# Optimization experiments

Hardware: AMD Instinct MI355X
Metric: run time of the kernel (lower is better)

The kernel has to match this reference:

```python
import jax, jax.numpy as jnp
import numpy as np

D = 128
RANK = 16
N_USER, N_PROD, N_CAT, N_BRAND = 100000, 100000, 1000, 2000
E_BEH, E_STR = 100000, 50000
NODE_TYPES = ['user', 'product', 'category', 'brand']
N_NODES = {'user': N_USER, 'product': N_PROD, 'category': N_CAT, 'brand': N_BRAND}
PHI = {'user': 0, 'product': 1, 'category': 2, 'brand': 3}
# (src_type, edge_name, dst_type, rel_idx, beta or None for structural)
EDGE_META = [
    ('user', 'view', 'product', 0, 0),
    ('user', 'cart', 'product', 1, 1),
    ('user', 'purchase', 'product', 2, 2),
    ('product', 'rev_view', 'user', 3, 0),
    ('product', 'rev_cart', 'user', 4, 1),
    ('product', 'rev_purchase', 'user', 5, 2),
    ('product', 'belongs_to', 'category', 6, None),
    ('category', 'contains', 'product', 7, None),
    ('product', 'producedBy', 'brand', 8, None),
    ('brand', 'brands', 'product', 9, None),
]


def setup_inputs() -> dict:
    key = jax.random.key(0)
    ks = iter(jax.random.split(key, 64))
    inp = {}
    for t in NODE_TYPES:
        inp['x_' + t] = jax.random.normal(next(ks), (N_NODES[t], D), jnp.float32)
    for (st, name, dt, ridx, beta) in EDGE_META:
        E = E_BEH if beta is not None else E_STR
        src = jax.random.randint(next(ks), (E,), 0, N_NODES[st], jnp.int32)
        dst = jax.random.randint(next(ks), (E,), 0, N_NODES[dt], jnp.int32)
        inp['ei_' + name] = jnp.stack([src, dst])
        if beta is None:
            inp['attr_' + name] = jax.random.randint(next(ks), (E,), 0, 3, jnp.int32)
    s = 0.05
    inp['W_base'] = jax.random.normal(next(ks), (D, D), jnp.float32) * s
    inp['A'] = jax.random.normal(next(ks), (4, D, RANK), jnp.float32) * s
    inp['B'] = jax.random.normal(next(ks), (4, D, RANK), jnp.float32) * s
    inp['rel_W'] = jax.random.normal(next(ks), (10, D), jnp.float32) * s
    inp['beh_W'] = jax.random.normal(next(ks), (4, D), jnp.float32) * s
    inp['a_att'] = jax.random.normal(next(ks), (4 * D,), jnp.float32) * s
    inp['ln_gamma'] = jnp.ones((D,), jnp.float32)
    inp['ln_beta'] = jnp.zeros((D,), jnp.float32)
    return inp


def _forward(x, eis, attrs, W_base, A, B, rel_W, beh_W, a_att, ln_gamma, ln_beta):
    a0, a1, a2, a3 = a_att[:D], a_att[D:2 * D], a_att[2 * D:3 * D], a_att[3 * D:]
    agg = {t: jnp.zeros((N_NODES[t], D), x['user'].dtype) for t in NODE_TYPES}
    for (src_t, name, dst_t, ridx, beta) in EDGE_META:
        ei = eis[name]
        src, dst = ei[0], ei[1]
        hs = x[src_t][src]            # [E, D] gather
        hd = x[dst_t][dst]            # [E, D] gather
        phi = PHI[src_t]
        if beta is not None:
            # uniform behavior beta: W = W_base + A_phi @ B_beta^T
            W = W_base + A[phi] @ B[beta].T
            msg = hs @ W.T
            hproj = hd @ W.T
            b_term = (beh_W[beta] * a3).sum()
        else:
            # per-edge behavior origin from edge_attr (clamped to {0,1,2})
            origin = jnp.clip(attrs[name].reshape(-1), 0, 2)
            mids = jnp.einsum('ei,bir->ebr', hs, B[:3])            # [E, 3, rank]
            mid = jnp.take_along_axis(mids, origin[:, None, None], axis=1)[:, 0, :]
            msg = hs @ W_base.T + mid @ A[phi].T
            hproj = hd @ W_base.T
            b_term = (beh_W[origin] * a3).sum(-1)                  # [E]
        r_scalar = (rel_W[ridx] * a2).sum()
        e = (msg * a0).sum(-1) + (hproj * a1).sum(-1) + r_scalar + b_term
        # destination-grouped softmax over edges
        n_dst = N_NODES[dst_t]
        m = jax.ops.segment_max(e, dst, num_segments=n_dst)
        ex = jnp.exp(e - m[dst])
        ssum = jax.ops.segment_sum(ex, dst, num_segments=n_dst)
        alpha = ex / (ssum[dst] + 1e-16)
        agg[dst_t] = agg[dst_t] + jax.ops.segment_sum(alpha[:, None] * msg, dst, num_segments=n_dst)
    outs = []
    for t in NODE_TYPES:
        h = agg[t]
        mu = h.mean(-1, keepdims=True)
        var = ((h - mu) ** 2).mean(-1, keepdims=True)
        hn = (h - mu) / jnp.sqrt(var + 1e-5) * ln_gamma + ln_beta
        outs.append(jax.nn.elu(hn + x[t]))   # residual: in_dim == out_dim
    return jnp.concatenate(outs, axis=0)     # [N_user+N_prod+N_cat+N_brand, D]


def reference(x_user, x_product, x_category, x_brand,
              ei_view, ei_cart, ei_purchase, ei_rev_view, ei_rev_cart, ei_rev_purchase,
              ei_belongs_to, ei_contains, ei_producedBy, ei_brands,
              attr_belongs_to, attr_contains, attr_producedBy, attr_brands,
              W_base, A, B, rel_W, beh_W, a_att, ln_gamma, ln_beta):
    x = {'user': x_user, 'product': x_product, 'category': x_category, 'brand': x_brand}
    eis = {'view': ei_view, 'cart': ei_cart, 'purchase': ei_purchase,
           'rev_view': ei_rev_view, 'rev_cart': ei_rev_cart, 'rev_purchase': ei_rev_purchase,
           'belongs_to': ei_belongs_to, 'contains': ei_contains,
           'producedBy': ei_producedBy, 'brands': ei_brands}
    attrs = {'belongs_to': attr_belongs_to, 'contains': attr_contains,
             'producedBy': attr_producedBy, 'brands': attr_brands}
    return _forward(x, eis, attrs, W_base, A, B, rel_W, beh_W, a_att, ln_gamma, ln_beta)
```

## Files before the change

### kernel.cpp

```cpp
#include <hip/hip_runtime.h>
#include <hip/hip_bf16.h>
#include <math.h>

#define D 128

#define NU 100000
#define NP 100000
#define NC 1000
#define NB 2000
#define NTOT 203000
#define EB 100000
#define ES 50000
#define ETOT 800000
#define NSEG 803000
#define NBLK 785

#define OFF_L    0
#define OFF_W0   6448000
#define OFF_BS   6451840
#define OFF_WT   7251856
#define OFF_AT   7268240
#define OFF_INT  7276432

__constant__ int c_srcT[10]   = {0,0,0,1,1,1,1,2,1,3};
__constant__ int c_phi [10]   = {0,0,0,1,1,1,1,2,1,3};
__constant__ int c_beta[10]   = {0,1,2,0,1,2,-1,-1,-1,-1};
__constant__ int c_E   [10]   = {EB,EB,EB,EB,EB,EB,ES,ES,ES,ES};
__constant__ int c_moff[10]   = {0,100000,200000,300000,400000,500000,600000,601000,701000,703000};

__constant__ int g_nGrp[4]    = {1,3,1,1};
__constant__ int g_Loff[4][3] = {{1600000,0,0},{0,3216000,4848000},{3200000,0,0},{4816000,0,0}};
__constant__ int g_ai[4][3]   = {{1,0,0},{0,2,3},{1,0,0},{1,0,0}};

#define K4_BU 782
#define K4_BP 1564
#define K4_BC 1572
#define K4_BT 1588

struct Ptrs {
    const float* x[4];
    const int*   ei[10];
    const int*   attr[4];
};

__device__ __forceinline__ void decode_et(int eflat, int& et, int& le) {
    if (eflat < 600000) { et = eflat / 100000; le = eflat - et * 100000; }
    else { int r = eflat - 600000; int q = r / 50000; et = 6 + q; le = r - q * 50000; }
}

__device__ __forceinline__ float qsum(float v) {
    v += __shfl_xor(v, 1, 64);
    v += __shfl_xor(v, 2, 64);
    v += __shfl_xor(v, 4, 64);
    v += __shfl_xor(v, 8, 64);
    return v;
}

__global__ void k0_tables(const float* __restrict__ Wb, const float* __restrict__ A,
                          const float* __restrict__ B, const float* __restrict__ behW,
                          const float* __restrict__ a_att,
                          float* __restrict__ w0, float* __restrict__ bs_out)
{
    __shared__ float a0[128];
    __shared__ float c0[128];
    __shared__ float g0[4][16];
    int t = threadIdx.x;
    if (t < 128) a0[t] = a_att[t];
    __syncthreads();
    if (t < 128) {
        float s0=0.f;
        for (int j=0;j<128;j++) s0 += Wb[j*128+t]*a0[j];
        c0[t]=s0;
    } else if (t < 192) {
        int q=t-128, p=q>>4, r=q&15;
        float s0=0.f;
        for (int i=0;i<128;i++) s0 += A[p*2048+i*16+r]*a0[i];
        g0[p][r]=s0;
    } else if (t < 196) {
        int b=t-192; float s=0.f;
        for (int i=0;i<128;i++) s += behW[b*128+i]*a_att[384+i];
        bs_out[b]=s;
    }
    __syncthreads();
    if (t < 128) {
        for (int et=0; et<10; ++et) {
            int phi=c_phi[et], beta=c_beta[et];
            if (beta >= 0) {
                float s0=c0[t];
                for (int r=0;r<16;r++) s0 += B[beta*2048+t*16+r]*g0[phi][r];
                w0[et*384+t]=s0; w0[et*384+128+t]=s0; w0[et*384+256+t]=s0;
            } else {
                for (int o=0;o<3;o++){
                    float s0=c0[t];
                    for (int r=0;r<16;r++) s0 += B[o*2048+t*16+r]*g0[phi][r];
                    w0[et*384+o*128+t]=s0;
                }
            }
        }
    }
}

__global__ __launch_bounds__(256) void ktrans(const float* __restrict__ Wb,
        const float* __restrict__ A, float* __restrict__ WbT, float* __restrict__ AT)
{
    int idx = blockIdx.x*256 + threadIdx.x;
    if (idx < 16384) { int i = idx>>7, j = idx&127; WbT[i*128+j] = Wb[j*128+i]; }
    int idx2 = idx - 16384;
    if (idx2 >= 0 && idx2 < 8192) {
        int p = idx2>>11, rem = idx2&2047, r = rem>>7, j = rem&127;
        AT[idx2] = A[p*2048 + j*16 + r];
    }
}

__global__ __launch_bounds__(256) void khist(Ptrs P, int* __restrict__ counts)
{
    int eflat = blockIdx.x*256 + threadIdx.x;
    if (eflat >= ETOT) return;
    int et, le; decode_et(eflat, et, le);
    int dst = P.ei[et][c_E[et] + le];
    atomicAdd(&counts[c_moff[et] + dst], 1);
}

__global__ __launch_bounds__(256) void kscan1(const int* __restrict__ cnt,
                                              int* __restrict__ st, int* __restrict__ bsums)
{
    __shared__ int lds[256];
    int t = threadIdx.x, b = blockIdx.x;
    int base = b*1024 + t*4;
    int v0 = (base   < NSEG) ? cnt[base]   : 0;
    int v1 = (base+1 < NSEG) ? cnt[base+1] : 0;
    int v2 = (base+2 < NSEG) ? cnt[base+2] : 0;
    int v3 = (base+3 < NSEG) ? cnt[base+3] : 0;
    int s = v0+v1+v2+v3;
    lds[t] = s; __syncthreads();
    for (int off=1; off<256; off<<=1){
        int xv = (t>=off) ? lds[t-off] : 0;
        __syncthreads();
        lds[t] += xv;
        __syncthreads();
    }
    int incl = lds[t];
    int p = incl - s;
    if (t==255) bsums[b] = incl;
    if (base   < NSEG) st[base]   = p; p += v0;
    if (base+1 < NSEG) st[base+1] = p; p += v1;
    if (base+2 < NSEG) st[base+2] = p; p += v2;
    if (base+3 < NSEG) st[base+3] = p;
}

__global__ __launch_bounds__(256) void kscan2(int* __restrict__ bsums)
{
    __shared__ int lds[256];
    int t = threadIdx.x;
    int base = t*4;
    int v0 = (base   < NBLK) ? bsums[base]   : 0;
    int v1 = (base+1 < NBLK) ? bsums[base+1] : 0;
    int v2 = (base+2 < NBLK) ? bsums[base+2] : 0;
    int v3 = (base+3 < NBLK) ? bsums[base+3] : 0;
    int s = v0+v1+v2+v3;
    lds[t] = s; __syncthreads();
    for (int off=1; off<256; off<<=1){
        int xv = (t>=off) ? lds[t-off] : 0;
        __syncthreads();
        lds[t] += xv;
        __syncthreads();
    }
    int p = lds[t] - s;
    if (base   < NBLK) bsums[base]   = p; p += v0;
    if (base+1 < NBLK) bsums[base+1] = p; p += v1;
    if (base+2 < NBLK) bsums[base+2] = p; p += v2;
    if (base+3 < NBLK) bsums[base+3] = p;
}

__global__ __launch_bounds__(256) void kscan3(int* __restrict__ st, const int* __restrict__ bsums)
{
    int t = threadIdx.x, b = blockIdx.x;
    int add = bsums[b];
    int base = b*1024 + t*4;
    #pragma unroll
    for (int j=0;j<4;j++)
        if (base+j < NSEG) st[base+j] += add;
}

__global__ __launch_bounds__(256) void kscatter(Ptrs P, int* __restrict__ st, int* __restrict__ srco)
{
    int eflat = blockIdx.x*256 + threadIdx.x;
    if (eflat >= ETOT) return;
    int et, le; decode_et(eflat, et, le);
    const int* ei = P.ei[et];
    int E = c_E[et];
    int src = ei[le], dst = ei[E+le];
    int o;
    if (et >= 6) { int a = P.attr[et-6][le]; o = min(max(a,0),2); }
    else o = c_beta[et];
    int pos = atomicAdd(&st[c_moff[et] + dst], 1);
    srco[pos] = src | (o<<17) | (et<<19);
}

__global__ __launch_bounds__(256) void kagg_beh(Ptrs P,
        const int* __restrict__ starts, const int* __restrict__ counts,
        const int* __restrict__ srco,
        const float* __restrict__ w0, const float* __restrict__ Bm,
        float* __restrict__ Sout, float* __restrict__ Lb, int nWaves)
{
    int lane = threadIdx.x & 63;
    int wv = (blockIdx.x * 256 + threadIdx.x) >> 6;
    int grp = lane >> 4, ln = lane & 15;

    for (int nid = wv; nid < NU + NP; nid += nWaves) {
        int T = (nid < NU) ? 0 : 1;
        int n0 = (T == 0) ? nid : nid - NU;
        int etBase = (T == 0) ? 3 : 0;
        const float* xs = P.x[1 - T];

        int sgA = c_moff[etBase] + n0;
        int cnt0 = counts[sgA],        cnt1 = counts[sgA+100000], cnt2 = counts[sgA+200000];
        int sa0  = starts[sgA]-cnt0,   sa1  = starts[sgA+100000]-cnt1, sa2 = starts[sgA+200000]-cnt2;
        int sv1 = (grp < cnt1) ? srco[sa1+grp] : 0;
        int sv2 = (grp < cnt2) ? srco[sa2+grp] : 0;
        float4 pA = make_float4(0.f,0.f,0.f,0.f), pB = pA;
        if (grp < cnt0) {
            int sv0 = srco[sa0+grp];
            const float* q = xs + (size_t)(sv0 & 0x1FFFF)*D + ln*8;
            pA = *(const float4*)q; pB = *(const float4*)(q+4);
        }

        float Stot[8] = {0,0,0,0,0,0,0,0};
        float Lq0=0.f, Lq1=0.f, Lq2=0.f, Lq3=0.f;

        for (int s=0; s<3; ++s) {
            int cnt = (s==0)?cnt0:((s==1)?cnt1:cnt2);
            int st0 = (s==0)?sa0:((s==1)?sa1:sa2);
            float4 cA = pA, cB = pB;
            pA = make_float4(0.f,0.f,0.f,0.f); pB = pA;
            if (s == 0) {
                if (grp < cnt1) {
                    const float* q = xs + (size_t)(sv1 & 0x1FFFF)*D + ln*8;
                    pA = *(const float4*)q; pB = *(const float4*)(q+4);
                }
            } else if (s == 1) {
                if (grp < cnt2) {
                    const float* q = xs + (size_t)(sv2 & 0x1FFFF)*D + ln*8;
                    pA = *(const float4*)q; pB = *(const float4*)(q+4);
                }
            }
            if (cnt == 0) continue;
            int et = etBase + s;
            const float* wq = w0 + et*384 + ln*8;
            float4 wA = *(const float4*)wq, wB = *(const float4*)(wq+4);

            float ssum = 0.f;
            float SA[8] = {0,0,0,0,0,0,0,0};

            for (int k0=0; k0<cnt; k0+=4) {
                bool act = (k0+grp) < cnt;
                if (k0 > 0) {
                    cA = make_float4(0.f,0.f,0.f,0.f); cB = cA;
                    if (act) {
                        int sv = srco[st0+k0+grp];
                        const float* q = xs + (size_t)(sv & 0x1FFFF)*D + ln*8;
                        cA = *(const float4*)q; cB = *(const float4*)(q+4);
                    }
                }
                float d = cA.x*wA.x + cA.y*wA.y + cA.z*wA.z + cA.w*wA.w
                        + cB.x*wB.x + cB.y*wB.y + cB.z*wB.z + cB.w*wB.w;
                d = qsum(d);
                float wg = act ? __expf(d) : 0.f;
                ssum += wg;
                SA[0]+=wg*cA.x; SA[1]+=wg*cA.y; SA[2]+=wg*cA.z; SA[3]+=wg*cA.w;
                SA[4]+=wg*cB.x; SA[5]+=wg*cB.y; SA[6]+=wg*cB.z; SA[7]+=wg*cB.w;
            }
            ssum += __shfl_xor(ssum, 16, 64);
            ssum += __shfl_xor(ssum, 32, 64);
            float inv = 1.f/(ssum + 1e-16f);
            #pragma unroll
            for (int j=0;j<8;j++){ SA[j] += __shfl_xor(SA[j],16,64); SA[j] += __shfl_xor(SA[j],32,64); }
            #pragma unroll
            for (int j=0;j<8;j++) Stot[j] += SA[j]*inv;

            const float* Bp = Bm + s*2048 + grp*4;
            float p0=0.f,p1=0.f,p2=0.f,p3=0.f;
            #pragma unroll
            for (int j=0;j<8;j++){
                float4 b4 = *(const float4*)(Bp + (ln*8+j)*16);
                float v = SA[j];
                p0+=v*b4.x; p1+=v*b4.y; p2+=v*b4.z; p3+=v*b4.w;
            }
            Lq0 += qsum(p0)*inv; Lq1 += qsum(p1)*inv;
            Lq2 += qsum(p2)*inv; Lq3 += qsum(p3)*inv;
        }

        if (grp == 0) {
            float* Srow = Sout + (size_t)nid*D + ln*8;
            *(float4*)Srow     = make_float4(Stot[0],Stot[1],Stot[2],Stot[3]);
            *(float4*)(Srow+4) = make_float4(Stot[4],Stot[5],Stot[6],Stot[7]);
        }
        if (ln < 4) {
            float v = (ln==0)?Lq0:((ln==1)?Lq1:((ln==2)?Lq2:Lq3));
            int loff = (T==0) ? 1600000 : 0;
            Lb[loff + (size_t)n0*16 + grp*4 + ln] = v;
        }
    }
}

__device__ __forceinline__ void str_seg_prod(int cnt, int st0, int hv,
        const int* __restrict__ srco, const float* __restrict__ xs,
        const float* __restrict__ wbase, float bs0, float bs1, float bs2,
        const float* __restrict__ Bm, int grp, int ln,
        float Stot[8], float* __restrict__ Lrow)
{
    if (cnt == 0) return;
    float ssum = 0.f;
    float SA[8]={0,0,0,0,0,0,0,0}, SB[8]={0,0,0,0,0,0,0,0}, SC[8]={0,0,0,0,0,0,0,0};
    int fa=0, fb=0, fc=0;

    for (int k0=0; k0<cnt; k0+=4) {
        bool act = (k0+grp) < cnt;
        int sv = (k0 == 0) ? hv : (act ? srco[st0+k0+grp] : 0);
        int o = (sv>>17)&3;
        float4 hA = make_float4(0.f,0.f,0.f,0.f), hB = hA;
        if (act) {
            const float* q = xs + (size_t)(sv & 0x1FFFF)*D + ln*8;
            hA = *(const float4*)q; hB = *(const float4*)(q+4);
        }
        const float* wq = wbase + o*128 + ln*8;
        float4 wA = *(const float4*)wq, wB = *(const float4*)(wq+4);
        float d = hA.x*wA.x + hA.y*wA.y + hA.z*wA.z + hA.w*wA.w
                + hB.x*wB.x + hB.y*wB.y + hB.z*wB.z + hB.w*wB.w;
        d = qsum(d);
        float wg = act ? __expf(d + ((o==0)?bs0:((o==1)?bs1:bs2))) : 0.f;
        ssum += wg;
        fa |= (int)(act && (o==0)); fb |= (int)(act && (o==1)); fc |= (int)(act && (o==2));
        float wg0=(o==0)?wg:0.f, wg1=(o==1)?wg:0.f, wg2=(o==2)?wg:0.f;
        #pragma unroll
        for (int j=0;j<8;j++){
            float hj = (j==0)?hA.x:(j==1)?hA.y:(j==2)?hA.z:(j==3)?hA.w:
                       (j==4)?hB.x:(j==5)?hB.y:(j==6)?hB.z:hB.w;
            SA[j] += wg0*hj; SB[j] += wg1*hj; SC[j] += wg2*hj;
        }
    }

    ssum += __shfl_xor(ssum, 16, 64);
    ssum += __shfl_xor(ssum, 32, 64);
    float inv = 1.f/(ssum + 1e-16f);

    int anyA = __any(fa), anyB = __any(fb), anyC = __any(fc);
    if (anyA) {
        #pragma unroll
        for (int j=0;j<8;j++){ SA[j] += __shfl_xor(SA[j],16,64); SA[j] += __shfl_xor(SA[j],32,64); }
    }
    if (anyB) {
        #pragma unroll
        for (int j=0;j<8;j++){ SB[j] += __shfl_xor(SB[j],16,64); SB[j] += __shfl_xor(SB[j],32,64); }
    }
    if (anyC) {
        #pragma unroll
        for (int j=0;j<8;j++){ SC[j] += __shfl_xor(SC[j],16,64); SC[j] += __shfl_xor(SC[j],32,64); }
    }
    #pragma unroll
    for (int j=0;j<8;j++) Stot[j] += (SA[j]+SB[j]+SC[j])*inv;

    float p0=0.f,p1=0.f,p2=0.f,p3=0.f;
    if (anyA) {
        const float* Bp = Bm + grp*4;
        #pragma unroll
        for (int j=0;j<8;j++){
            float4 b4 = *(const float4*)(Bp + (ln*8+j)*16);
            float v = SA[j];
            p0+=v*b4.x; p1+=v*b4.y; p2+=v*b4.z; p3+=v*b4.w;
        }
    }
    if (anyB) {
        const float* Bp = Bm + 2048 + grp*4;
        #pragma unroll
        for (int j=0;j<8;j++){
            float4 b4 = *(const float4*)(Bp + (ln*8+j)*16);
            float v = SB[j];
            p0+=v*b4.x; p1+=v*b4.y; p2+=v*b4.z; p3+=v*b4.w;
        }
    }
    if (anyC) {
        const float* Bp = Bm + 4096 + grp*4;
        #pragma unroll
        for (int j=0;j<8;j++){
            float4 b4 = *(const float4*)(Bp + (ln*8+j)*16);
            float v = SC[j];
            p0+=v*b4.x; p1+=v*b4.y; p2+=v*b4.z; p3+=v*b4.w;
        }
    }
    p0 = qsum(p0)*inv; p1 = qsum(p1)*inv; p2 = qsum(p2)*inv; p3 = qsum(p3)*inv;
    if (ln < 4) {
        float v = (ln==0)?p0:((ln==1)?p1:((ln==2)?p2:p3));
        Lrow[grp*4 + ln] = v;
    }
}

__global__ __launch_bounds__(256) void kagg_str(Ptrs P,
        const int* __restrict__ starts, const int* __restrict__ counts,
        const int* __restrict__ srco,
        const float* __restrict__ w0, const float* __restrict__ bs,
        const float* __restrict__ Bm,
        float* __restrict__ Sout, float* __restrict__ Lb, int nWaves)
{
    int lane = threadIdx.x & 63;
    int wv = (blockIdx.x * 256 + threadIdx.x) >> 6;
    int grp = lane >> 4, ln = lane & 15;
    float bs0 = bs[0], bs1 = bs[1], bs2 = bs[2];

    for (int id = wv; id < NP + NC + NB; id += nWaves) {
        if (id < NP) {
            int n0 = id;
            int seg7 = 601000 + n0, seg9 = 703000 + n0;
            int cnt7 = counts[seg7], cnt9 = counts[seg9];
            if ((cnt7 | cnt9) == 0) continue;
            int st7 = starts[seg7] - cnt7, st9 = starts[seg9] - cnt9;
            int hv7 = (grp < cnt7) ? srco[st7+grp] : 0;
            int hv9 = (grp < cnt9) ? srco[st9+grp] : 0;

            float Stot[8] = {0,0,0,0,0,0,0,0};
            str_seg_prod(cnt7, st7, hv7, srco, P.x[2], w0 + 7*384,
                         bs0, bs1, bs2, Bm, grp, ln, Stot,
                         Lb + 3216000 + (size_t)n0*16);
            str_seg_prod(cnt9, st9, hv9, srco, P.x[3], w0 + 9*384,
                         bs0, bs1, bs2, Bm, grp, ln, Stot,
                         Lb + 4848000 + (size_t)n0*16);

            if (grp == 0) {
                float* Srow = Sout + (size_t)(100000+n0)*D + ln*8;
                float4 a = *(const float4*)Srow, b = *(const float4*)(Srow+4);
                *(float4*)Srow     = make_float4(a.x+Stot[0],a.y+Stot[1],a.z+Stot[2],a.w+Stot[3]);
                *(float4*)(Srow+4) = make_float4(b.x+Stot[4],b.y+Stot[5],b.z+Stot[6],b.w+Stot[7]);
            }
        } else {
            int T = (id < NP+NC) ? 2 : 3;
            int n0 = (T==2) ? (id-NP) : (id-(NP+NC));
            int et = (T==2) ? 6 : 8;
            int outRow = (T==2) ? (200000+n0) : (201000+n0);
            int seg = c_moff[et] + n0;
            int cnt = counts[seg];
            int st0 = starts[seg] - cnt;
            const float* xs = P.x[1];
            const float* wbase = w0 + et*384;

            float ssum = 0.f;
            float SA[8]={0,0,0,0,0,0,0,0}, SB[8]={0,0,0,0,0,0,0,0}, SC[8]={0,0,0,0,0,0,0,0};
            int fa=0, fb=0, fc=0;

            int sv = 0;
            float4 hA = make_float4(0.f,0.f,0.f,0.f), hB = hA;
            if (grp < cnt) {
                sv = srco[st0+grp];
                const float* q = xs + (size_t)(sv & 0x1FFFF)*D + ln*8;
                hA = *(const float4*)q; hB = *(const float4*)(q+4);
            }
            for (int k0=0; k0<cnt; k0+=4) {
                int svn = 0;
                float4 nA = make_float4(0.f,0.f,0.f,0.f), nB = nA;
                if (k0+4+grp < cnt) {
                    svn = srco[st0+k0+4+grp];
                    const float* q = xs + (size_t)(svn & 0x1FFFF)*D + ln*8;
                    nA = *(const float4*)q; nB = *(const float4*)(q+4);
                }
                bool act = (k0+grp) < cnt;
                int o = (sv>>17)&3;
                const float* wq = wbase + o*128 + ln*8;
                float4 wA = *(const float4*)wq, wB = *(const float4*)(wq+4);
                float d = hA.x*wA.x + hA.y*wA.y + hA.z*wA.z + hA.w*wA.w
                        + hB.x*wB.x + hB.y*wB.y + hB.z*wB.z + hB.w*wB.w;
                d = qsum(d);
                float wg = act ? __expf(d + ((o==0)?bs0:((o==1)?bs1:bs2))) : 0.f;
                ssum += wg;
                fa |= (int)(act && (o==0)); fb |= (int)(act && (o==1)); fc |= (int)(act && (o==2));
                float wg0=(o==0)?wg:0.f, wg1=(o==1)?wg:0.f, wg2=(o==2)?wg:0.f;
                #pragma unroll
                for (int j=0;j<8;j++){
                    float hj = (j==0)?hA.x:(j==1)?hA.y:(j==2)?hA.z:(j==3)?hA.w:
                               (j==4)?hB.x:(j==5)?hB.y:(j==6)?hB.z:hB.w;
                    SA[j] += wg0*hj; SB[j] += wg1*hj; SC[j] += wg2*hj;
                }
                sv = svn; hA = nA; hB = nB;
            }

            ssum += __shfl_xor(ssum, 16, 64);
            ssum += __shfl_xor(ssum, 32, 64);
            float inv = 1.f/(ssum + 1e-16f);

            int anyA = __any(fa), anyB = __any(fb), anyC = __any(fc);
            if (anyA) {
                #pragma unroll
                for (int j=0;j<8;j++){ SA[j] += __shfl_xor(SA[j],16,64); SA[j] += __shfl_xor(SA[j],32,64); }
            }
            if (anyB) {
                #pragma unroll
                for (int j=0;j<8;j++){ SB[j] += __shfl_xor(SB[j],16,64); SB[j] += __shfl_xor(SB[j],32,64); }
            }
            if (anyC) {
                #pragma unroll
                for (int j=0;j<8;j++){ SC[j] += __shfl_xor(SC[j],16,64); SC[j] += __shfl_xor(SC[j],32,64); }
            }
            float Stot[8];
            #pragma unroll
            for (int j=0;j<8;j++) Stot[j] = (SA[j]+SB[j]+SC[j])*inv;

            float p0=0.f,p1=0.f,p2=0.f,p3=0.f;
            if (anyA) {
                const float* Bp = Bm + grp*4;
                #pragma unroll
                for (int j=0;j<8;j++){
                    float4 b4 = *(const float4*)(Bp + (ln*8+j)*16);
                    float v = SA[j];
                    p0+=v*b4.x; p1+=v*b4.y; p2+=v*b4.z; p3+=v*b4.w;
                }
            }
            if (anyB) {
                const float* Bp = Bm + 2048 + grp*4;
                #pragma unroll
                for (int j=0;j<8;j++){
                    float4 b4 = *(const float4*)(Bp + (ln*8+j)*16);
                    float v = SB[j];
                    p0+=v*b4.x; p1+=v*b4.y; p2+=v*b4.z; p3+=v*b4.w;
                }
            }
            if (anyC) {
                const float* Bp = Bm + 4096 + grp*4;
                #pragma unroll
                for (int j=0;j<8;j++){
                    float4 b4 = *(const float4*)(Bp + (ln*8+j)*16);
                    float v = SC[j];
                    p0+=v*b4.x; p1+=v*b4.y; p2+=v*b4.z; p3+=v*b4.w;
                }
            }
            p0 = qsum(p0)*inv; p1 = qsum(p1)*inv; p2 = qsum(p2)*inv; p3 = qsum(p3)*inv;

            int loff = (T==2) ? 3200000 : 4816000;
            if (ln < 4) {
                float v = (ln==0)?p0:((ln==1)?p1:((ln==2)?p2:p3));
                Lb[loff + (size_t)n0*16 + grp*4 + ln] = v;
            }
            if (grp == 0) {
                float* Srow = Sout + (size_t)outRow*D + ln*8;
                *(float4*)Srow     = make_float4(Stot[0],Stot[1],Stot[2],Stot[3]);
                *(float4*)(Srow+4) = make_float4(Stot[4],Stot[5],Stot[6],Stot[7]);
            }
        }
    }
}

__global__ __launch_bounds__(512, 1) void k4_final(Ptrs P,
        const float* __restrict__ WbT, const float* __restrict__ AT,
        const float* __restrict__ Lb,
        const float* __restrict__ gamma, const float* __restrict__ lbeta,
        float* __restrict__ out)
{
    __shared__ float st[128*132];
    __shared__ float wt[128*128];
    __shared__ float lt[128*52];
    int t = threadIdx.x;
    int b = blockIdx.x;
    int T, lb;
    if (b < K4_BU)      { T=0; lb=b; }
    else if (b < K4_BP) { T=1; lb=b-K4_BU; }
    else if (b < K4_BC) { T=2; lb=b-K4_BP; }
    else                { T=3; lb=b-K4_BC; }
    int r0 = lb*128;
    int rowStart = (T==0)?0:((T==1)?100000:((T==2)?200000:201000));
    int nRows    = (T==0)?NU:((T==1)?NP:((T==2)?NC:NB));
    const float* x = P.x[T];
    int nPairs = g_nGrp[T];

    for (int idx=t; idx<4096; idx+=512)
        *(float4*)&wt[idx*4] = *(const float4*)&WbT[idx*4];
    for (int idx=t; idx<4096; idx+=512){
        int r = idx>>5, i4 = idx&31;
        int lr = r0 + r;
        float4 v = (lr < nRows) ? *(const float4*)&out[(size_t)(rowStart+lr)*D + i4*4]
                                : make_float4(0.f,0.f,0.f,0.f);
        *(float4*)&st[r*132 + i4*4] = v;
    }
    for (int pi=0; pi<nPairs; ++pi){
        int lo = g_Loff[T][pi];
        int r = t>>2, q = t&3;
        int lr = r0 + r;
        float4 v = (lr < nRows) ? *(const float4*)&Lb[lo + (size_t)lr*16 + q*4]
                                : make_float4(0.f,0.f,0.f,0.f);
        *(float4*)&lt[r*52 + pi*16 + q*4] = v;
    }
    __syncthreads();

    int cg = t & 15, rg = t >> 4;
    float acc[4][8];
    #pragma unroll
    for (int a=0;a<4;a++)
        #pragma unroll
        for (int c=0;c<8;c++) acc[a][c]=0.f;

    for (int i4=0; i4<32; ++i4){
        float4 sv0 = *(const float4*)&st[(rg*4+0)*132 + i4*4];
        float4 sv1 = *(const float4*)&st[(rg*4+1)*132 + i4*4];
        float4 sv2 = *(const float4*)&st[(rg*4+2)*132 + i4*4];
        float4 sv3 = *(const float4*)&st[(rg*4+3)*132 + i4*4];
        #pragma unroll
        for (int q=0;q<4;q++){
            float4 wA = *(const float4*)&wt[(i4*4+q)*128 + cg*4];
            float4 wB = *(const float4*)&wt[(i4*4+q)*128 + 64 + cg*4];
            float sq[4];
            sq[0] = (q==0)?sv0.x:(q==1)?sv0.y:(q==2)?sv0.z:sv0.w;
            sq[1] = (q==0)?sv1.x:(q==1)?sv1.y:(q==2)?sv1.z:sv1.w;
            sq[2] = (q==0)?sv2.x:(q==1)?sv2.y:(q==2)?sv2.z:sv2.w;
            sq[3] = (q==0)?sv3.x:(q==1)?sv3.y:(q==2)?sv3.z:sv3.w;
            #pragma unroll
            for (int rr=0;rr<4;rr++){
                acc[rr][0] += sq[rr]*wA.x;
                acc[rr][1] += sq[rr]*wA.y;
                acc[rr][2] += sq[rr]*wA.z;
                acc[rr][3] += sq[rr]*wA.w;
                acc[rr][4] += sq[rr]*wB.x;
                acc[rr][5] += sq[rr]*wB.y;
                acc[rr][6] += sq[rr]*wB.z;
                acc[rr][7] += sq[rr]*wB.w;
            }
        }
    }

    for (int pi=0; pi<nPairs; ++pi){
        int ai = g_ai[T][pi];
        const float* Ap = AT + ai*2048;
        #pragma unroll 4
        for (int r=0;r<16;++r){
            float4 aA = *(const float4*)&Ap[r*128 + cg*4];
            float4 aB = *(const float4*)&Ap[r*128 + 64 + cg*4];
            float lv[4];
            #pragma unroll
            for (int rr=0;rr<4;rr++) lv[rr] = lt[(rg*4+rr)*52 + pi*16 + r];
            #pragma unroll
            for (int rr=0;rr<4;rr++){
                acc[rr][0] += lv[rr]*aA.x;
                acc[rr][1] += lv[rr]*aA.y;
                acc[rr][2] += lv[rr]*aA.z;
                acc[rr][3] += lv[rr]*aA.w;
                acc[rr][4] += lv[rr]*aB.x;
                acc[rr][5] += lv[rr]*aB.y;
                acc[rr][6] += lv[rr]*aB.z;
                acc[rr][7] += lv[rr]*aB.w;
            }
        }
    }

    int jA = cg*4, jB = 64 + cg*4;
    float4 gA = *(const float4*)&gamma[jA], gB = *(const float4*)&gamma[jB];
    float4 bA = *(const float4*)&lbeta[jA], bB = *(const float4*)&lbeta[jB];
    float gv[8] = {gA.x,gA.y,gA.z,gA.w,gB.x,gB.y,gB.z,gB.w};
    float bv[8] = {bA.x,bA.y,bA.z,bA.w,bB.x,bB.y,bB.z,bB.w};

    #pragma unroll
    for (int rr=0;rr<4;rr++){
        int lr = r0 + rg*4 + rr;
        float lsum=0.f, lsq=0.f;
        #pragma unroll
        for (int c=0;c<8;c++){ lsum += acc[rr][c]; lsq += acc[rr][c]*acc[rr][c]; }
        #pragma unroll
        for (int mm=1; mm<16; mm<<=1){ lsum += __shfl_xor(lsum,mm,64); lsq += __shfl_xor(lsq,mm,64); }
        if (lr >= nRows) continue;
        float mu = lsum*(1.f/128.f);
        float var = lsq*(1.f/128.f) - mu*mu;
        float rstd = rsqrtf(var + 1e-5f);
        const float* xr = x + (size_t)lr*D;
        float4 xA = *(const float4*)(xr+jA), xB = *(const float4*)(xr+jB);
        float xv[8] = {xA.x,xA.y,xA.z,xA.w,xB.x,xB.y,xB.z,xB.w};
        float ov[8];
        #pragma unroll
        for (int c=0;c<8;c++){
            float hn = (acc[rr][c]-mu)*rstd*gv[c] + bv[c];
            float z = hn + xv[c];
            ov[c] = z > 0.f ? z : expm1f(z);
        }
        float* orow = out + (size_t)(rowStart+lr)*D;
        *(float4*)(orow+jA) = make_float4(ov[0],ov[1],ov[2],ov[3]);
        *(float4*)(orow+jB) = make_float4(ov[4],ov[5],ov[6],ov[7]);
    }
}

extern "C" void kernel_launch(void* const* d_in, const int* in_sizes, int n_in,
                              void* d_out, int out_size, void* d_ws, size_t ws_size,
                              hipStream_t stream)
{
    (void)in_sizes; (void)n_in; (void)out_size; (void)ws_size;
    Ptrs P;
    P.x[0] = (const float*)d_in[0];
    P.x[1] = (const float*)d_in[1];
    P.x[2] = (const float*)d_in[2];
    P.x[3] = (const float*)d_in[3];
    P.ei[0] = (const int*)d_in[4];
    P.ei[1] = (const int*)d_in[5];
    P.ei[2] = (const int*)d_in[6];
    P.ei[3] = (const int*)d_in[7];
    P.ei[4] = (const int*)d_in[8];
    P.ei[5] = (const int*)d_in[9];
    P.ei[6] = (const int*)d_in[10];
    P.attr[0] = (const int*)d_in[11];
    P.ei[7] = (const int*)d_in[12];
    P.attr[1] = (const int*)d_in[13];
    P.ei[8] = (const int*)d_in[14];
    P.attr[2] = (const int*)d_in[15];
    P.ei[9] = (const int*)d_in[16];
    P.attr[3] = (const int*)d_in[17];
    const float* Wb    = (const float*)d_in[18];
    const float* A     = (const float*)d_in[19];
    const float* B     = (const float*)d_in[20];
    const float* behW  = (const float*)d_in[22];
    const float* a_att = (const float*)d_in[23];
    const float* gamma = (const float*)d_in[24];
    const float* lbeta = (const float*)d_in[25];
    float* wsf = (float*)d_ws;
    float* out = (float*)d_out;

    int* ip     = (int*)(wsf + OFF_INT);
    int* counts = ip;
    int* starts = ip + 803000;
    int* srco   = ip + 1606000;
    int* bsums  = (int*)wsf;

    hipMemsetAsync(counts, 0, (size_t)NSEG*sizeof(int), stream);
    hipMemsetAsync(wsf + OFF_L, 0, (size_t)6448000*sizeof(float), stream);

    k0_tables<<<1, 256, 0, stream>>>(Wb, A, B, behW, a_att, wsf+OFF_W0, wsf+OFF_BS);
    ktrans<<<96, 256, 0, stream>>>(Wb, A, wsf+OFF_WT, wsf+OFF_AT);
    khist<<<3125, 256, 0, stream>>>(P, counts);
    kscan1<<<NBLK, 256, 0, stream>>>(counts, starts, bsums);
    kscan2<<<1, 256, 0, stream>>>(bsums);
    kscan3<<<NBLK, 256, 0, stream>>>(starts, bsums);
    kscatter<<<3125, 256, 0, stream>>>(P, starts, srco);

    kagg_beh<<<4096, 256, 0, stream>>>(P, starts, counts, srco,
                                       wsf+OFF_W0, B, out, wsf+OFF_L, 4096*4);
    kagg_str<<<1024, 256, 0, stream>>>(P, starts, counts, srco,
                                       wsf+OFF_W0, wsf+OFF_BS, B, out, wsf+OFF_L, 1024*4);

    k4_final<<<K4_BT, 512, 0, stream>>>(P, wsf+OFF_WT, wsf+OFF_AT, wsf+OFF_L,
                                        gamma, lbeta, out);
}
```

Before: 872.8 us.

## Software-pipeline segment metadata and head-index loads in behavioral aggregation

Prefetches the counts, starts and first source index of the next one or two nodes in kagg_beh across loop iterations. This hides the dependent index-load latency chain that sits before each node's feature gather. It also shrinks the L-buffer memset to skip the range kagg_beh fully overwrites. The cost is extra live registers, which may lower occupancy, and it relies on that region being fully written.

Result: no change. 859.9 us (-1.5%).

```diff
diff --git a/kernel.cpp b/kernel.cpp
--- a/kernel.cpp
+++ b/kernel.cpp
@@ -14,6 +14,7 @@
 #define ETOT 800000
 #define NSEG 803000
 #define NBLK 785
+#define NTOTB 200000
 
 #define OFF_L    0
 #define OFF_W0   6448000
@@ -207,22 +208,58 @@
     int wv = (blockIdx.x * 256 + threadIdx.x) >> 6;
     int grp = lane >> 4, ln = lane & 15;
 
-    for (int nid = wv; nid < NU + NP; nid += nWaves) {
+    if (wv >= NTOTB) return;
+
+    int a0,a1,a2,b0,b1,b2;
+    {
+        int nid = wv;
+        int sg = ((nid < NU) ? (300000 + nid) : (nid - NU));
+        a0 = counts[sg];         a1 = counts[sg+100000];  a2 = counts[sg+200000];
+        b0 = starts[sg];         b1 = starts[sg+100000];  b2 = starts[sg+200000];
+    }
+    int h0=0, h1=0, h2=0;
+    if (grp < a0) h0 = srco[b0-a0+grp];
+    if (grp < a1) h1 = srco[b1-a1+grp];
+    if (grp < a2) h2 = srco[b2-a2+grp];
+    int cc0=0,cc1=0,cc2=0, ce0=0,ce1=0,ce2=0;
+    if (wv + nWaves < NTOTB) {
+        int nid = wv + nWaves;
+        int sg = ((nid < NU) ? (300000 + nid) : (nid - NU));
+        cc0 = counts[sg];        cc1 = counts[sg+100000]; cc2 = counts[sg+200000];
+        ce0 = starts[sg];        ce1 = starts[sg+100000]; ce2 = starts[sg+200000];
+    }
+
+    for (int nid = wv; nid < NTOTB; nid += nWaves) {
         int T = (nid < NU) ? 0 : 1;
         int n0 = (T == 0) ? nid : nid - NU;
         int etBase = (T == 0) ? 3 : 0;
         const float* xs = P.x[1 - T];
 
-        int sgA = c_moff[etBase] + n0;
-        int cnt0 = counts[sgA],        cnt1 = counts[sgA+100000], cnt2 = counts[sgA+200000];
-        int sa0  = starts[sgA]-cnt0,   sa1  = starts[sgA+100000]-cnt1, sa2 = starts[sgA+200000]-cnt2;
-        int sv1 = (grp < cnt1) ? srco[sa1+grp] : 0;
-        int sv2 = (grp < cnt2) ? srco[sa2+grp] : 0;
+        int cnt0 = a0, cnt1 = a1, cnt2 = a2;
+        int sa0 = b0-a0, sa1 = b1-a1, sa2 = b2-a2;
+        int sv1 = h1, sv2 = h2;
+
+        int f0=0,f1=0,f2=0, g0=0,g1=0,g2=0;
+        {
+            int nid2 = nid + 2*nWaves;
+            if (nid2 < NTOTB) {
+                int sg = ((nid2 < NU) ? (300000 + nid2) : (nid2 - NU));
+                f0 = counts[sg];     f1 = counts[sg+100000]; f2 = counts[sg+200000];
+                g0 = starts[sg];     g1 = starts[sg+100000]; g2 = starts[sg+200000];
+            }
+        }
+
         float4 pA = make_float4(0.f,0.f,0.f,0.f), pB = pA;
         if (grp < cnt0) {
-            int sv0 = srco[sa0+grp];
-            const float* q = xs + (size_t)(sv0 & 0x1FFFF)*D + ln*8;
+            const float* q = xs + (size_t)(h0 & 0x1FFFF)*D + ln*8;
             pA = *(const float4*)q; pB = *(const float4*)(q+4);
+        }
+
+        int i0=0, i1=0, i2=0;
+        if (nid + nWaves < NTOTB) {
+            if (grp < cc0) i0 = srco[ce0-cc0+grp];
+            if (grp < cc1) i1 = srco[ce1-cc1+grp];
+            if (grp < cc2) i2 = srco[ce2-cc2+grp];
         }
 
         float Stot[8] = {0,0,0,0,0,0,0,0};
@@ -300,6 +337,12 @@
             int loff = (T==0) ? 1600000 : 0;
             Lb[loff + (size_t)n0*16 + grp*4 + ln] = v;
         }
+
+        a0 = cc0; a1 = cc1; a2 = cc2;
+        b0 = ce0; b1 = ce1; b2 = ce2;
+        cc0 = f0; cc1 = f1; cc2 = f2;
+        ce0 = g0; ce1 = g1; ce2 = g2;
+        h0 = i0; h1 = i1; h2 = i2;
     }
 }
 
@@ -721,7 +764,7 @@
     int* bsums  = (int*)wsf;
 
     hipMemsetAsync(counts, 0, (size_t)NSEG*sizeof(int), stream);
-    hipMemsetAsync(wsf + OFF_L, 0, (size_t)6448000*sizeof(float), stream);
+    hipMemsetAsync(wsf + 3216000, 0, (size_t)(6448000-3216000)*sizeof(float), stream);
 
     k0_tables<<<1, 256, 0, stream>>>(Wb, A, B, behW, a_att, wsf+OFF_W0, wsf+OFF_BS);
     ktrans<<<96, 256, 0, stream>>>(Wb, A, wsf+OFF_WT, wsf+OFF_AT);
```
